# Optimization experiments

Hardware: AMD Instinct MI355X
Metric: run time of the kernel (lower is better)

Reference implementation:

```python
import jax, jax.numpy as jnp
import numpy as np

B, C, N, OUT, K = 8, 64, 4096, 64, 20
KNN_SKIP = 6   # knn computed on channels 6: (as in x[:, 6:])
BN_EPS = 1e-5
NEG_SLOPE = 0.2


def setup_inputs() -> dict:
    key = jax.random.key(0)
    k1, k2, k3, k4 = jax.random.split(key, 4)
    x = jax.random.normal(k1, (B, C, N), dtype=jnp.float32)
    W = jax.random.normal(k2, (OUT, 2 * C), dtype=jnp.float32) * (1.0 / np.sqrt(2 * C))
    gamma = jax.random.normal(k3, (OUT,), dtype=jnp.float32) * 0.1 + 1.0
    beta = jax.random.normal(k4, (OUT,), dtype=jnp.float32) * 0.1
    return {"x": x, "W": W, "gamma": gamma, "beta": beta}


def _knn_idx(xk, k):
    # xk: (B, Ck, N). pairwise_distance[b,i,j] = -||x_i - x_j||^2
    sq = jnp.sum(xk * xk, axis=1)                       # (B, N)
    inner = jnp.einsum('bcn,bcm->bnm', xk, xk)          # (B, N, N)
    pd = 2.0 * inner - sq[:, :, None] - sq[:, None, :]  # (B, N, N)
    return jax.lax.top_k(pd, k)[1]                      # (B, N, k) int32


def reference(x, W, gamma, beta):
    idx = _knn_idx(x[:, KNN_SKIP:, :], K)               # (B, N, K)
    xt = jnp.transpose(x, (0, 2, 1))                    # (B, N, C)
    # gather neighbor features: (B, N, K, C)
    neigh = jnp.take_along_axis(xt[:, None, :, :], idx[:, :, :, None], axis=2)
    center = jnp.broadcast_to(xt[:, :, None, :], neigh.shape)
    edge = jnp.concatenate([neigh - center, center], axis=-1)  # (B, N, K, 2C)
    # 1x1 conv (no bias): contract channel dim -> (B, OUT, N, K)
    y = jnp.einsum('bnkc,oc->bonk', edge, W)
    # BatchNorm2d (training-mode batch stats, biased variance)
    mean = jnp.mean(y, axis=(0, 2, 3), keepdims=True)
    var = jnp.var(y, axis=(0, 2, 3), keepdims=True)
    y = (y - mean) * jax.lax.rsqrt(var + BN_EPS)
    y = y * gamma[None, :, None, None] + beta[None, :, None, None]
    # LeakyReLU(0.2)
    y = jnp.where(y >= 0, y, NEG_SLOPE * y)
    # max over k neighbors -> (B, OUT, N)
    return jnp.max(y, axis=-1)
```

## Files before the change

kernel.cpp:

```cpp
#include <hip/hip_runtime.h>
#include <cstdint>
#include <cstddef>

#define BB 8
#define CC 64
#define NN 4096
#define OO 64
#define KK 20
#define KC 58
#define HC 29
#define KSKIP 6
#define NSPLIT 8
#define JS 512
#define TIDX 8
#define REC 16
#define FBCAP 96
#define BN_EPS 1e-5f
#define NEG 0.2f
#define NEGINF (-3.402823466e38f)
#define M_TOTAL 655360.0f
#define HPAD 4

#define MED3F(a, b, c) __builtin_amdgcn_fmed3f((a), (b), (c))


__global__ void k_sq(const float* __restrict__ x, float* __restrict__ h) {
  int n = blockIdx.x * 256 + threadIdx.x;
  int b = n >> 12;
  int nn = n & (NN - 1);
  const float* xp = x + ((size_t)b * CC + KSKIP) * NN + nn;
  float s = 0.f;
#pragma unroll
  for (int c = 0; c < KC; ++c) {
    float v = xp[(size_t)c * NN];
    s = fmaf(v, v, s);
  }
  h[n] = 0.5f * s;
}

#define RIP(tv, e)                                   \
  do {                                               \
    float _e = (e);                                  \
    tv[19] = MED3F(tv[18], tv[19], _e);              \
    tv[18] = MED3F(tv[17], tv[18], _e);              \
    tv[17] = MED3F(tv[16], tv[17], _e);              \
    tv[16] = MED3F(tv[15], tv[16], _e);              \
    tv[15] = MED3F(tv[14], tv[15], _e);              \
    tv[14] = MED3F(tv[13], tv[14], _e);              \
    tv[13] = MED3F(tv[12], tv[13], _e);              \
    tv[12] = MED3F(tv[11], tv[12], _e);              \
    tv[11] = MED3F(tv[10], tv[11], _e);              \
    tv[10] = MED3F(tv[9],  tv[10], _e);              \
    tv[9]  = MED3F(tv[8],  tv[9],  _e);              \
    tv[8]  = MED3F(tv[7],  tv[8],  _e);              \
    tv[7]  = MED3F(tv[6],  tv[7],  _e);              \
    tv[6]  = MED3F(tv[5],  tv[6],  _e);              \
    tv[5]  = MED3F(tv[4],  tv[5],  _e);              \
    tv[4]  = MED3F(tv[3],  tv[4],  _e);              \
    tv[3]  = MED3F(tv[2],  tv[3],  _e);              \
    tv[2]  = MED3F(tv[1],  tv[2],  _e);              \
    tv[1]  = MED3F(tv[0],  tv[1],  _e);              \
    tv[0]  = fmaxf(tv[0], _e);                       \
  } while (0)

#define RIPX8(tv, ti, e, jj)                                                  \
  do {                                                                        \
    float _e = (e);                                                           \
    int _j = (jj);                                                            \
    bool c0 = _e > tv[0], c1 = _e > tv[1], c2 = _e > tv[2], c3 = _e > tv[3];  \
    bool c4 = _e > tv[4], c5 = _e > tv[5], c6 = _e > tv[6], c7 = _e > tv[7];  \
    tv[7] = MED3F(tv[6], tv[7], _e); ti[7] = c6 ? ti[6] : (c7 ? _j : ti[7]);  \
    tv[6] = MED3F(tv[5], tv[6], _e); ti[6] = c5 ? ti[5] : (c6 ? _j : ti[6]);  \
    tv[5] = MED3F(tv[4], tv[5], _e); ti[5] = c4 ? ti[4] : (c5 ? _j : ti[5]);  \
    tv[4] = MED3F(tv[3], tv[4], _e); ti[4] = c3 ? ti[3] : (c4 ? _j : ti[4]);  \
    tv[3] = MED3F(tv[2], tv[3], _e); ti[3] = c2 ? ti[2] : (c3 ? _j : ti[3]);  \
    tv[2] = MED3F(tv[1], tv[2], _e); ti[2] = c1 ? ti[1] : (c2 ? _j : ti[2]);  \
    tv[1] = MED3F(tv[0], tv[1], _e); ti[1] = c0 ? ti[0] : (c1 ? _j : ti[1]);  \
    tv[0] = fmaxf(tv[0], _e);        ti[0] = c0 ? _j : ti[0];                 \
  } while (0)

#define DIST8P(jq)                                                    \
  float a0 = 0.f, a1 = 0.f, a2 = 0.f, a3 = 0.f;                       \
  float a4 = 0.f, a5 = 0.f, a6 = 0.f, a7 = 0.f;                       \
  _Pragma("unroll")                                                   \
  for (int cc = 0; cc < HC; ++cc) {                                   \
    float4 x0 = *(const float4*)(ltp + cc * 64 + (jq) * 8);           \
    float4 x1 = *(const float4*)(ltp + cc * 64 + (jq) * 8 + 4);       \
    float xic = xi[cc];                                               \
    a0 = fmaf(xic, x0.x, a0); a1 = fmaf(xic, x0.y, a1);               \
    a2 = fmaf(xic, x0.z, a2); a3 = fmaf(xic, x0.w, a3);               \
    a4 = fmaf(xic, x1.x, a4); a5 = fmaf(xic, x1.y, a5);               \
    a6 = fmaf(xic, x1.z, a6); a7 = fmaf(xic, x1.w, a7);               \
  }                                                                   \
  a0 += __shfl_xor(a0, 1); a1 += __shfl_xor(a1, 1);                   \
  a2 += __shfl_xor(a2, 1); a3 += __shfl_xor(a3, 1);                   \
  a4 += __shfl_xor(a4, 1); a5 += __shfl_xor(a5, 1);                   \
  a6 += __shfl_xor(a6, 1); a7 += __shfl_xor(a7, 1);                   \
  float4 hA = *(const float4*)(lh + (jq) * 8 + half4);                \
  float d0 = (half4 ? a4 : a0) - hA.x;                                \
  float d1 = (half4 ? a5 : a1) - hA.y;                                \
  float d2 = (half4 ? a6 : a2) - hA.z;                                \
  float d3 = (half4 ? a7 : a3) - hA.w;

#define STAGE_TILE(jbase)                                             \
  __syncthreads();                                                    \
  for (int f = t; f < KC * 16; f += 256) {                            \
    int c = f >> 4, q = f & 15;                                       \
    float4 v = *(const float4*)(xb + c * NN + (jbase) + q * 4);       \
    *(float4*)(ltile + c * 64 + q * 4 + (c >= HC ? HPAD : 0)) = v;    \
  }                                                                   \
  if (t < 64) lh[t] = hg[b * NN + (jbase) + t];                       \
  __syncthreads();

__global__ __launch_bounds__(256, 4) void k_knnA(const float* __restrict__ x,
                                                 const float* __restrict__ hg,
                                                 float* __restrict__ candvx) {
  __shared__ float ltile[KC * 64 + HPAD];
  __shared__ float lh[64];
  int t = threadIdx.x;
  int l = t & 63;
  int w = t >> 6;
  int half = l & 1;
  int half4 = half * 4;
  int bidx = blockIdx.x;
  int b = bidx >> 8;
  int itile = (bidx >> 3) & 31;
  int split = bidx & 7;
  int i = itile * 128 + w * 32 + (l >> 1);
  const float* xb = x + ((size_t)b * CC + KSKIP) * NN;
  const float* ltp = ltile + half * (HC * 64 + HPAD);

  float xi[HC];
#pragma unroll
  for (int cc = 0; cc < HC; ++cc) xi[cc] = xb[(half * HC + cc) * NN + i];

  float tv[TIDX];
  int ti[TIDX];
#pragma unroll
  for (int s = 0; s < TIDX; ++s) { tv[s] = NEGINF; ti[s] = -1; }

#pragma unroll 1
  for (int jt = 0; jt < JS / 64; ++jt) {
    int jbase = split * JS + jt * 64;
    STAGE_TILE(jbase)
#pragma unroll 1
    for (int jq = 0; jq < 8; ++jq) {
      DIST8P(jq)
      int j0 = jbase + jq * 8 + half4;
      RIPX8(tv, ti, d0, j0 + 0); RIPX8(tv, ti, d1, j0 + 1);
      RIPX8(tv, ti, d2, j0 + 2); RIPX8(tv, ti, d3, j0 + 3);
    }
  }

  float ov[TIDX];
  int oi[TIDX];
#pragma unroll
  for (int s = 0; s < TIDX; ++s) ov[s] = __shfl_xor(tv[s], 1);
#pragma unroll
  for (int s = 0; s < TIDX; ++s) oi[s] = __shfl_xor(ti[s], 1);
#pragma unroll
  for (int s = 0; s < TIDX; ++s) { RIPX8(tv, ti, ov[s], oi[s]); }

  if (!half) {
    float* cv = candvx + (((size_t)(b * NN + i)) * NSPLIT + split) * REC;
    *(float4*)(cv + 0) = make_float4(tv[0], tv[1], tv[2], tv[3]);
    *(float4*)(cv + 4) = make_float4(tv[4], tv[5], tv[6], tv[7]);
    int* cvi = (int*)(cv + TIDX);
    *(int4*)(cvi + 0) = make_int4(ti[0], ti[1], ti[2], ti[3]);
    *(int4*)(cvi + 4) = make_int4(ti[4], ti[5], ti[6], ti[7]);
  }
}

__global__ void k_final(const float* __restrict__ candvx, int* __restrict__ idxk,
                        float* __restrict__ thrv, int* __restrict__ fbl,
                        int* __restrict__ fbcnt) {
  int qi = blockIdx.x * 256 + threadIdx.x;
  const float* cv = candvx + (size_t)qi * NSPLIT * REC;
  float tv[KK];
#pragma unroll
  for (int s = 0; s < KK; ++s) tv[s] = NEGINF;
  float v7max = NEGINF;
#pragma unroll 1
  for (int sp = 0; sp < NSPLIT; ++sp) {
    const float* r = cv + sp * REC;
#pragma unroll
    for (int s = 0; s < TIDX; ++s) { RIP(tv, r[s]); }
    v7max = fmaxf(v7max, r[TIDX - 1]);
  }
  float thr = tv[19];
  thrv[qi] = thr;
  int* op = idxk + (size_t)qi * KK;
  int m = 0;
  bool fb = (v7max >= thr);
  if (!fb) {
#pragma unroll 1
    for (int sp = 0; sp < NSPLIT; ++sp) {
      const float* r = cv + sp * REC;
      const int* ri = (const int*)(r + TIDX);
#pragma unroll
      for (int s = 0; s < TIDX; ++s) {
        float v = r[s];
        if (v > thr) {
          if (m < KK) op[m] = ri[s];
          ++m;
        }
      }
    }
    if (m >= KK) fb = true;
  }
  if (fb) {
    int p = atomicAdd(fbcnt, 1);
    fbl[p] = qi;
    return;
  }
  int need = KK - m;
  int last = -1;
#pragma unroll 1
  for (int r2 = 0; r2 < need; ++r2) {
    int best = 0x7fffffff;
#pragma unroll 1
    for (int sp = 0; sp < NSPLIT; ++sp) {
      const float* r = cv + sp * REC;
      const int* ri = (const int*)(r + TIDX);
#pragma unroll
      for (int s = 0; s < TIDX; ++s) {
        if (r[s] == thr) {
          int jx = ri[s];
          if (jx > last && jx < best) best = jx;
        }
      }
    }
    op[m + r2] = best;
    last = best;
  }
}

__global__ __launch_bounds__(256) void k_fb(const float* __restrict__ x,
                                            const float* __restrict__ hg,
                                            const float* __restrict__ thrv,
                                            const int* __restrict__ fbl,
                                            const int* __restrict__ fbcnt,
                                            int* __restrict__ idxk) {
  __shared__ float xiA[HC];
  __shared__ float xiB[HC];
  __shared__ float db[FBCAP * 2];
  __shared__ int cnt;
  int t = threadIdx.x;
  int nfb = *fbcnt;
  if (nfb > BB * NN) nfb = BB * NN;
#pragma unroll 1
  for (int q = blockIdx.x; q < nfb; q += gridDim.x) {
    int qi = fbl[q];
    int b = qi >> 12;
    int i = qi & (NN - 1);
    const float* xb = x + ((size_t)b * CC + KSKIP) * NN;
    if (t < HC) xiA[t] = xb[t * NN + i];
    else if (t < 2 * HC) xiB[t - HC] = xb[(size_t)t * NN + i];
    if (t == 0) cnt = 0;
    __syncthreads();
    float thr = thrv[qi];
#pragma unroll 1
    for (int j = t; j < NN; j += 256) {
      float s1 = 0.f, s2 = 0.f;
#pragma unroll
      for (int cc = 0; cc < HC; ++cc) s1 = fmaf(xiA[cc], xb[cc * NN + j], s1);
#pragma unroll
      for (int cc = 0; cc < HC; ++cc) s2 = fmaf(xiB[cc], xb[(HC + cc) * NN + j], s2);
      float d = (s1 + s2) - hg[b * NN + j];
      if (d >= thr) {
        int p = atomicAdd(&cnt, 1);
        if (p < FBCAP) { db[p * 2] = d; db[p * 2 + 1] = __int_as_float(j); }
      }
    }
    __syncthreads();
    if (t == 0) {
      int n = cnt;
      if (n > FBCAP) n = FBCAP;
      int* op = idxk + (size_t)qi * KK;
      for (int r = 0; r < KK; ++r) {
        float bd = NEGINF;
        int bj = 0x7fffffff;
        int be = -1;
        for (int e = 0; e < n; ++e) {
          float d = db[e * 2];
          int jx = __float_as_int(db[e * 2 + 1]);
          if (d > bd || (d == bd && jx < bj)) { bd = d; bj = jx; be = e; }
        }
        op[r] = bj;
        if (be >= 0) db[be * 2] = NEGINF;
      }
    }
    __syncthreads();
  }
}

__global__ void k_uv(const float* __restrict__ x, const float* __restrict__ W,
                     float* __restrict__ ut, float* __restrict__ vt) {
  __shared__ float w1[64 * 65];
  __shared__ float wd[64 * 65];
  __shared__ float xs[64 * 72];
  int t = threadIdx.x;
  int b = blockIdx.x >> 6;
  int nbase = (blockIdx.x & 63) * 64;

  for (int f = t; f < 4096; f += 256) {
    int o = f >> 6, c = f & 63;
    float a = W[o * 128 + c];
    float b2 = W[o * 128 + 64 + c];
    w1[c * 65 + o] = a;
    wd[c * 65 + o] = b2 - a;
  }
  for (int f = t; f < 1024; f += 256) {
    int c = f >> 4, q = f & 15;
    float4 v = *(const float4*)(x + ((size_t)b * CC + c) * NN + nbase + q * 4);
    *(float4*)(xs + c * 72 + q * 4) = v;
  }
  __syncthreads();

  int o = t & 63, w = t >> 6;
  float4 au[4], av[4];
#pragma unroll
  for (int nq = 0; nq < 4; ++nq) {
    au[nq] = make_float4(0.f, 0.f, 0.f, 0.f);
    av[nq] = make_float4(0.f, 0.f, 0.f, 0.f);
  }
#pragma unroll 4
  for (int c = 0; c < 64; ++c) {
    float w1v = w1[c * 65 + o];
    float wdv = wd[c * 65 + o];
#pragma unroll
    for (int nq = 0; nq < 4; ++nq) {
      float4 xv = *(const float4*)(xs + c * 72 + w * 16 + nq * 4);
      au[nq].x = fmaf(w1v, xv.x, au[nq].x);
      au[nq].y = fmaf(w1v, xv.y, au[nq].y);
      au[nq].z = fmaf(w1v, xv.z, au[nq].z);
      au[nq].w = fmaf(w1v, xv.w, au[nq].w);
      av[nq].x = fmaf(wdv, xv.x, av[nq].x);
      av[nq].y = fmaf(wdv, xv.y, av[nq].y);
      av[nq].z = fmaf(wdv, xv.z, av[nq].z);
      av[nq].w = fmaf(wdv, xv.w, av[nq].w);
    }
  }
#pragma unroll
  for (int nq = 0; nq < 4; ++nq) {
    int n = nbase + w * 16 + nq * 4;
    size_t base = ((size_t)b * NN + n) * OO + o;
    ut[base + 0 * OO] = au[nq].x;
    ut[base + 1 * OO] = au[nq].y;
    ut[base + 2 * OO] = au[nq].z;
    ut[base + 3 * OO] = au[nq].w;
    vt[base + 0 * OO] = av[nq].x;
    vt[base + 1 * OO] = av[nq].y;
    vt[base + 2 * OO] = av[nq].z;
    vt[base + 3 * OO] = av[nq].w;
  }
}

__global__ void k_stats(const float* __restrict__ ut, const float* __restrict__ vt,
                        const int* __restrict__ idxk, float* __restrict__ gsum,
                        float* __restrict__ gsqs) {
  __shared__ float red[2][4][64];
  int t = threadIdx.x;
  int o = t & 63, w = t >> 6;
  int b = blockIdx.x >> 6;
  int nbase = (blockIdx.x & 63) * 64 + w * 16;
  const float* up = ut + (size_t)b * NN * OO;
  float s = 0.f, s2 = 0.f;
#pragma unroll 1
  for (int nn2 = 0; nn2 < 16; ++nn2) {
    int n = nbase + nn2;
    float vv = vt[((size_t)b * NN + n) * OO + o];
    const int* ip = idxk + ((size_t)b * NN + n) * KK;
    int4 q0 = *(const int4*)(ip + 0);
    int4 q1 = *(const int4*)(ip + 4);
    int4 q2 = *(const int4*)(ip + 8);
    int4 q3 = *(const int4*)(ip + 12);
    int4 q4 = *(const int4*)(ip + 16);
#define ACC(j)                                  \
    {                                           \
      float u = up[(size_t)(j) * OO + o];       \
      float yy = u + vv;                        \
      s += yy;                                  \
      s2 = fmaf(yy, yy, s2);                    \
    }
    ACC(q0.x) ACC(q0.y) ACC(q0.z) ACC(q0.w)
    ACC(q1.x) ACC(q1.y) ACC(q1.z) ACC(q1.w)
    ACC(q2.x) ACC(q2.y) ACC(q2.z) ACC(q2.w)
    ACC(q3.x) ACC(q3.y) ACC(q3.z) ACC(q3.w)
    ACC(q4.x) ACC(q4.y) ACC(q4.z) ACC(q4.w)
#undef ACC
  }
  red[0][w][o] = s;
  red[1][w][o] = s2;
  __syncthreads();
  if (w == 0) {
    float ts = red[0][0][o] + red[0][1][o] + red[0][2][o] + red[0][3][o];
    float t2 = red[1][0][o] + red[1][1][o] + red[1][2][o] + red[1][3][o];
    atomicAdd(&gsum[o], ts);
    atomicAdd(&gsqs[o], t2);
  }
}

__global__ void k_bn(const float* __restrict__ gsum, const float* __restrict__ gsqs,
                     const float* __restrict__ gamma, const float* __restrict__ beta,
                     float* __restrict__ AB) {
  int o = threadIdx.x;
  float mean = gsum[o] * (1.f / M_TOTAL);
  float var = gsqs[o] * (1.f / M_TOTAL) - mean * mean;
  float A = gamma[o] / sqrtf(var + BN_EPS);
  AB[o] = A;
  AB[64 + o] = beta[o] - mean * A;
}

__global__ void k_out(const float* __restrict__ ut, const float* __restrict__ vt,
                      const int* __restrict__ idxk, const float* __restrict__ AB,
                      float* __restrict__ outp) {
  __shared__ float lt[64 * 65];
  int t = threadIdx.x;
  int o = t & 63, w = t >> 6;
  int b = blockIdx.x >> 6;
  int nb = (blockIdx.x & 63) * 64;
  float A = AB[o], Bs = AB[64 + o];
  const float* up = ut + (size_t)b * NN * OO;
#pragma unroll 1
  for (int nn2 = 0; nn2 < 16; ++nn2) {
    int nl = w * 16 + nn2;
    int n = nb + nl;
    float vv = vt[((size_t)b * NN + n) * OO + o];
    const int* ip = idxk + ((size_t)b * NN + n) * KK;
    int4 q0 = *(const int4*)(ip + 0);
    int4 q1 = *(const int4*)(ip + 4);
    int4 q2 = *(const int4*)(ip + 8);
    int4 q3 = *(const int4*)(ip + 12);
    int4 q4 = *(const int4*)(ip + 16);
    float m = NEGINF;
#define STEP(j)                                   \
    {                                             \
      float u = up[(size_t)(j) * OO + o];         \
      float y = fmaf(A, u + vv, Bs);              \
      y = fmaxf(y, NEG * y);                      \
      m = fmaxf(m, y);                            \
    }
    STEP(q0.x) STEP(q0.y) STEP(q0.z) STEP(q0.w)
    STEP(q1.x) STEP(q1.y) STEP(q1.z) STEP(q1.w)
    STEP(q2.x) STEP(q2.y) STEP(q2.z) STEP(q2.w)
    STEP(q3.x) STEP(q3.y) STEP(q3.z) STEP(q3.w)
    STEP(q4.x) STEP(q4.y) STEP(q4.z) STEP(q4.w)
#undef STEP
    lt[nl * 65 + o] = m;
  }
  __syncthreads();
  int oo = t >> 2, part = t & 3;
#pragma unroll
  for (int mq = 0; mq < 4; ++mq) {
    int n0 = part * 16 + mq * 4;
    float4 vvv;
    vvv.x = lt[(n0 + 0) * 65 + oo];
    vvv.y = lt[(n0 + 1) * 65 + oo];
    vvv.z = lt[(n0 + 2) * 65 + oo];
    vvv.w = lt[(n0 + 3) * 65 + oo];
    *(float4*)(outp + ((size_t)b * OO + oo) * NN + nb + n0) = vvv;
  }
}

extern "C" void kernel_launch(void* const* d_in, const int* in_sizes, int n_in,
                              void* d_out, int out_size, void* d_ws, size_t ws_size,
                              hipStream_t stream) {
  const float* x = (const float*)d_in[0];
  const float* W = (const float*)d_in[1];
  const float* gamma = (const float*)d_in[2];
  const float* beta = (const float*)d_in[3];
  float* outp = (float*)d_out;
  char* ws = (char*)d_ws;

  const size_t NQ = (size_t)BB * NN;
  size_t off = 0;
  float* hg = (float*)(ws + off); off += NQ * 4;
  float* thrv = (float*)(ws + off); off += NQ * 4;
  int* idxk = (int*)(ws + off); off += NQ * KK * 4;
  int* fbcnt = (int*)(ws + off); off += 256;
  int* fbl = (int*)(ws + off); off += NQ * 4;
  float* gsum = (float*)(ws + off); off += 256;
  float* gsqs = (float*)(ws + off); off += 256;
  float* AB = (float*)(ws + off); off += 512;
  char* region = ws + off;
  float* candvx = (float*)region;
  float* ut = (float*)region;
  float* vt = (float*)(region + NQ * OO * 4);

  k_sq<<<BB * NN / 256, 256, 0, stream>>>(x, hg);
  k_knnA<<<BB * 32 * NSPLIT, 256, 0, stream>>>(x, hg, candvx);
  hipMemsetAsync(fbcnt, 0, 4, stream);
  k_final<<<BB * NN / 256, 256, 0, stream>>>(candvx, idxk, thrv, fbl, fbcnt);
  k_fb<<<256, 256, 0, stream>>>(x, hg, thrv, fbl, fbcnt, idxk);
  k_uv<<<BB * 64, 256, 0, stream>>>(x, W, ut, vt);
  hipMemsetAsync(gsum, 0, 512, stream);
  k_stats<<<BB * 64, 256, 0, stream>>>(ut, vt, idxk, gsum, gsqs);
  k_bn<<<1, 64, 0, stream>>>(gsum, gsqs, gamma, beta, AB);
  k_out<<<BB * 64, 256, 0, stream>>>(ut, vt, idxk, AB, outp);
}
```

Measured before the change: 629.9 us.

## Precompute neighbor max in stats pass, transpose candidate layout, shrink small-kernel blocks

k_stats now also records the per-point, per-channel max of u+v over the K neighbors. k_out uses it directly when the BN scale A is non-negative, because the affine map followed by LeakyReLU is monotone in that case, so the second neighbor gather is skipped. The kNN candidate buffer moves from per-query records to structure-of-arrays planes so k_final reads coalesced. k_sq and k_final launch with 64-thread blocks instead of 256. This costs an extra NQ*OO float buffer and its write traffic, and the negative-A path keeps a slower non-unrolled gather.

Result: no change. 624.5 us (-0.9%).

```diff
diff --git a/kernel.cpp b/kernel.cpp
--- a/kernel.cpp
+++ b/kernel.cpp
@@ -13,7 +13,7 @@
 #define NSPLIT 8
 #define JS 512
 #define TIDX 8
-#define REC 16
+#define NQ2 32768
 #define FBCAP 96
 #define BN_EPS 1e-5f
 #define NEG 0.2f
@@ -25,7 +25,7 @@
 
 
 __global__ void k_sq(const float* __restrict__ x, float* __restrict__ h) {
-  int n = blockIdx.x * 256 + threadIdx.x;
+  int n = blockIdx.x * 64 + threadIdx.x;
   int b = n >> 12;
   int nn = n & (NN - 1);
   const float* xp = x + ((size_t)b * CC + KSKIP) * NN + nn;
@@ -112,6 +112,8 @@
   if (t < 64) lh[t] = hg[b * NN + (jbase) + t];                       \
   __syncthreads();
 
+#define PLANE ((size_t)NSPLIT * NQ2)
+
 __global__ __launch_bounds__(256, 4) void k_knnA(const float* __restrict__ x,
                                                  const float* __restrict__ hg,
                                                  float* __restrict__ candvx) {
@@ -162,30 +164,30 @@
   for (int s = 0; s < TIDX; ++s) { RIPX8(tv, ti, ov[s], oi[s]); }
 
   if (!half) {
-    float* cv = candvx + (((size_t)(b * NN + i)) * NSPLIT + split) * REC;
-    *(float4*)(cv + 0) = make_float4(tv[0], tv[1], tv[2], tv[3]);
-    *(float4*)(cv + 4) = make_float4(tv[4], tv[5], tv[6], tv[7]);
-    int* cvi = (int*)(cv + TIDX);
-    *(int4*)(cvi + 0) = make_int4(ti[0], ti[1], ti[2], ti[3]);
-    *(int4*)(cvi + 4) = make_int4(ti[4], ti[5], ti[6], ti[7]);
+    float* pl = candvx + (size_t)split * NQ2 + (size_t)(b * NN + i);
+#pragma unroll
+    for (int s = 0; s < TIDX; ++s) pl[(size_t)s * PLANE] = tv[s];
+#pragma unroll
+    for (int s = 0; s < TIDX; ++s) pl[(size_t)(s + TIDX) * PLANE] = __int_as_float(ti[s]);
   }
 }
 
 __global__ void k_final(const float* __restrict__ candvx, int* __restrict__ idxk,
                         float* __restrict__ thrv, int* __restrict__ fbl,
                         int* __restrict__ fbcnt) {
-  int qi = blockIdx.x * 256 + threadIdx.x;
-  const float* cv = candvx + (size_t)qi * NSPLIT * REC;
+  int qi = blockIdx.x * 64 + threadIdx.x;
+  const float* pv = candvx + qi;
+#define CV(s, sp) pv[((size_t)(s) * NSPLIT + (sp)) * NQ2]
+#define CI(s, sp) __float_as_int(pv[((size_t)((s) + TIDX) * NSPLIT + (sp)) * NQ2])
   float tv[KK];
 #pragma unroll
   for (int s = 0; s < KK; ++s) tv[s] = NEGINF;
   float v7max = NEGINF;
 #pragma unroll 1
   for (int sp = 0; sp < NSPLIT; ++sp) {
-    const float* r = cv + sp * REC;
-#pragma unroll
-    for (int s = 0; s < TIDX; ++s) { RIP(tv, r[s]); }
-    v7max = fmaxf(v7max, r[TIDX - 1]);
+#pragma unroll
+    for (int s = 0; s < TIDX; ++s) { RIP(tv, CV(s, sp)); }
+    v7max = fmaxf(v7max, CV(TIDX - 1, sp));
   }
   float thr = tv[19];
   thrv[qi] = thr;
@@ -195,13 +197,11 @@
   if (!fb) {
 #pragma unroll 1
     for (int sp = 0; sp < NSPLIT; ++sp) {
-      const float* r = cv + sp * REC;
-      const int* ri = (const int*)(r + TIDX);
 #pragma unroll
       for (int s = 0; s < TIDX; ++s) {
-        float v = r[s];
+        float v = CV(s, sp);
         if (v > thr) {
-          if (m < KK) op[m] = ri[s];
+          if (m < KK) op[m] = CI(s, sp);
           ++m;
         }
       }
@@ -220,12 +220,10 @@
     int best = 0x7fffffff;
 #pragma unroll 1
     for (int sp = 0; sp < NSPLIT; ++sp) {
-      const float* r = cv + sp * REC;
-      const int* ri = (const int*)(r + TIDX);
 #pragma unroll
       for (int s = 0; s < TIDX; ++s) {
-        if (r[s] == thr) {
-          int jx = ri[s];
+        if (CV(s, sp) == thr) {
+          int jx = CI(s, sp);
           if (jx > last && jx < best) best = jx;
         }
       }
@@ -233,6 +231,8 @@
     op[m + r2] = best;
     last = best;
   }
+#undef CV
+#undef CI
 }
 
 __global__ __launch_bounds__(256) void k_fb(const float* __restrict__ x,
@@ -358,7 +358,7 @@
 
 __global__ void k_stats(const float* __restrict__ ut, const float* __restrict__ vt,
                         const int* __restrict__ idxk, float* __restrict__ gsum,
-                        float* __restrict__ gsqs) {
+                        float* __restrict__ gsqs, float* __restrict__ mxv) {
   __shared__ float red[2][4][64];
   int t = threadIdx.x;
   int o = t & 63, w = t >> 6;
@@ -376,12 +376,14 @@
     int4 q2 = *(const int4*)(ip + 8);
     int4 q3 = *(const int4*)(ip + 12);
     int4 q4 = *(const int4*)(ip + 16);
+    float mx = NEGINF;
 #define ACC(j)                                  \
     {                                           \
       float u = up[(size_t)(j) * OO + o];       \
       float yy = u + vv;                        \
       s += yy;                                  \
       s2 = fmaf(yy, yy, s2);                    \
+      mx = fmaxf(mx, yy);                       \
     }
     ACC(q0.x) ACC(q0.y) ACC(q0.z) ACC(q0.w)
     ACC(q1.x) ACC(q1.y) ACC(q1.z) ACC(q1.w)
@@ -389,6 +391,7 @@
     ACC(q3.x) ACC(q3.y) ACC(q3.z) ACC(q3.w)
     ACC(q4.x) ACC(q4.y) ACC(q4.z) ACC(q4.w)
 #undef ACC
+    mxv[((size_t)b * NN + n) * OO + o] = mx;
   }
   red[0][w][o] = s;
   red[1][w][o] = s2;
@@ -413,8 +416,8 @@
 }
 
 __global__ void k_out(const float* __restrict__ ut, const float* __restrict__ vt,
-                      const int* __restrict__ idxk, const float* __restrict__ AB,
-                      float* __restrict__ outp) {
+                      const int* __restrict__ idxk, const float* __restrict__ mxv,
+                      const float* __restrict__ AB, float* __restrict__ outp) {
   __shared__ float lt[64 * 65];
   int t = threadIdx.x;
   int o = t & 63, w = t >> 6;
@@ -426,28 +429,25 @@
   for (int nn2 = 0; nn2 < 16; ++nn2) {
     int nl = w * 16 + nn2;
     int n = nb + nl;
-    float vv = vt[((size_t)b * NN + n) * OO + o];
-    const int* ip = idxk + ((size_t)b * NN + n) * KK;
-    int4 q0 = *(const int4*)(ip + 0);
-    int4 q1 = *(const int4*)(ip + 4);
-    int4 q2 = *(const int4*)(ip + 8);
-    int4 q3 = *(const int4*)(ip + 12);
-    int4 q4 = *(const int4*)(ip + 16);
-    float m = NEGINF;
-#define STEP(j)                                   \
-    {                                             \
-      float u = up[(size_t)(j) * OO + o];         \
-      float y = fmaf(A, u + vv, Bs);              \
-      y = fmaxf(y, NEG * y);                      \
-      m = fmaxf(m, y);                            \
-    }
-    STEP(q0.x) STEP(q0.y) STEP(q0.z) STEP(q0.w)
-    STEP(q1.x) STEP(q1.y) STEP(q1.z) STEP(q1.w)
-    STEP(q2.x) STEP(q2.y) STEP(q2.z) STEP(q2.w)
-    STEP(q3.x) STEP(q3.y) STEP(q3.z) STEP(q3.w)
-    STEP(q4.x) STEP(q4.y) STEP(q4.z) STEP(q4.w)
-#undef STEP
-    lt[nl * 65 + o] = m;
+    float y;
+    if (A >= 0.f) {
+      float mx = mxv[((size_t)b * NN + n) * OO + o];
+      float z = fmaf(A, mx, Bs);
+      y = fmaxf(z, NEG * z);
+    } else {
+      float vv = vt[((size_t)b * NN + n) * OO + o];
+      const int* ip = idxk + ((size_t)b * NN + n) * KK;
+      float m = NEGINF;
+#pragma unroll 1
+      for (int e = 0; e < KK; ++e) {
+        float u = up[(size_t)ip[e] * OO + o];
+        float z = fmaf(A, u + vv, Bs);
+        z = fmaxf(z, NEG * z);
+        m = fmaxf(m, z);
+      }
+      y = m;
+    }
+    lt[nl * 65 + o] = y;
   }
   __syncthreads();
   int oo = t >> 2, part = t & 3;
@@ -487,15 +487,16 @@
   float* candvx = (float*)region;
   float* ut = (float*)region;
   float* vt = (float*)(region + NQ * OO * 4);
-
-  k_sq<<<BB * NN / 256, 256, 0, stream>>>(x, hg);
+  float* mxv = (float*)(region + 2 * NQ * OO * 4);
+
+  k_sq<<<BB * NN / 64, 64, 0, stream>>>(x, hg);
   k_knnA<<<BB * 32 * NSPLIT, 256, 0, stream>>>(x, hg, candvx);
   hipMemsetAsync(fbcnt, 0, 4, stream);
-  k_final<<<BB * NN / 256, 256, 0, stream>>>(candvx, idxk, thrv, fbl, fbcnt);
+  k_final<<<BB * NN / 64, 64, 0, stream>>>(candvx, idxk, thrv, fbl, fbcnt);
   k_fb<<<256, 256, 0, stream>>>(x, hg, thrv, fbl, fbcnt, idxk);
   k_uv<<<BB * 64, 256, 0, stream>>>(x, W, ut, vt);
   hipMemsetAsync(gsum, 0, 512, stream);
-  k_stats<<<BB * 64, 256, 0, stream>>>(ut, vt, idxk, gsum, gsqs);
+  k_stats<<<BB * 64, 256, 0, stream>>>(ut, vt, idxk, gsum, gsqs, mxv);
   k_bn<<<1, 64, 0, stream>>>(gsum, gsqs, gamma, beta, AB);
-  k_out<<<BB * 64, 256, 0, stream>>>(ut, vt, idxk, AB, outp);
-}
+  k_out<<<BB * 64, 256, 0, stream>>>(ut, vt, idxk, mxv, AB, outp);
+}
```
